# Kernel tuning notes

Hardware: AMD Instinct MI355X
Metric: run time of the kernel (lower is better)

The kernel has to match this reference:

```python
import jax, jax.numpy as jnp
import numpy as np

B, D_IN, D_H, W_RANK, U_RANK = 8192, 1024, 2048, 256, 256


def setup_inputs() -> dict:
    key = jax.random.key(0)
    ks = jax.random.split(key, 6)
    return {
        "input": jax.random.normal(ks[0], (B, D_IN), dtype=jnp.float32),
        "state": jax.random.normal(ks[1], (B, D_H), dtype=jnp.float32),
        "W1": 0.1 * jax.random.normal(ks[2], (W_RANK, D_IN), dtype=jnp.float32),
        "W2": 0.1 * jax.random.normal(ks[3], (D_H, W_RANK), dtype=jnp.float32),
        "U1": 0.1 * jax.random.normal(ks[4], (U_RANK, D_H), dtype=jnp.float32),
        "U2": 0.1 * jax.random.normal(ks[5], (D_H, U_RANK), dtype=jnp.float32),
        "bias_gate": jnp.ones((1, D_H), dtype=jnp.float32),
        "bias_update": jnp.ones((1, D_H), dtype=jnp.float32),
        "zeta": 1.0 * jnp.ones((1, 1), dtype=jnp.float32),
        "nu": -4.0 * jnp.ones((1, 1), dtype=jnp.float32),
    }


def reference(input, state, W1, W2, U1, U2, bias_gate, bias_update, zeta, nu):
    # Low-rank projections: Wx = x @ W1^T @ W2^T ; Uh = h @ U1^T @ U2^T
    wx = jnp.einsum("bi,ri->br", input, W1)          # [B, wRank]
    wx = jnp.einsum("br,hr->bh", wx, W2)             # [B, H]
    uh = jnp.einsum("bh,rh->br", state, U1)          # [B, uRank]
    uh = jnp.einsum("br,hr->bh", uh, U2)             # [B, H]
    pre = wx + uh                                     # shared pre-activation
    z = jax.nn.sigmoid(pre + bias_gate)               # gate (sigmoid)
    h_cand = jnp.tanh(pre + bias_update)              # update (tanh)
    # h_t = z*h_{t-1} + (sigmoid(zeta)*(1-z) + sigmoid(nu)) * h_cand
    new_h = z * state + (jax.nn.sigmoid(zeta) * (1.0 - z) + jax.nn.sigmoid(nu)) * h_cand
    return new_h
```

## Files before the change

### kernel.cpp

```cpp
#include <hip/hip_runtime.h>
#include <hip/hip_fp16.h>
#include <cstdint>
#include <cstddef>


typedef _Float16 half8 __attribute__((ext_vector_type(8)));
typedef float f32x4 __attribute__((ext_vector_type(4)));

#define DIN 1024
#define DH 2048
#define RK 256
#define RBLD 768
#define OFF_W1H 0
#define OFF_U1H 262144
#define OFF_W2H 786432
#define OFF_U2H 1310720

__device__ __forceinline__ half8 cvt8(const float4 a, const float4 b) {
  half8 h;
  h[0] = (_Float16)a.x; h[1] = (_Float16)a.y; h[2] = (_Float16)a.z; h[3] = (_Float16)a.w;
  h[4] = (_Float16)b.x; h[5] = (_Float16)b.y; h[6] = (_Float16)b.z; h[7] = (_Float16)b.w;
  return h;
}

__device__ __forceinline__ void gload16(const _Float16* g, _Float16* lds) {
  __builtin_amdgcn_global_load_lds(
      (const __attribute__((address_space(1))) unsigned*)g,
      (__attribute__((address_space(3))) unsigned*)lds, 16, 0, 0);
}

__global__ __launch_bounds__(256)
void fgrnn_prep(const float* __restrict__ W1, const float* __restrict__ U1,
                const float* __restrict__ W2, const float* __restrict__ U2,
                _Float16* __restrict__ wb) {
  const int q = blockIdx.x * 256 + threadIdx.x;
  const float* src;
  int rel;
  if (q < 65536) { src = W1; rel = q; }
  else if (q < 196608) { src = U1; rel = q - 65536; }
  else if (q < 327680) { src = W2; rel = q - 196608; }
  else { src = U2; rel = q - 327680; }
  const float4 v = reinterpret_cast<const float4*>(src)[rel];
  union { _Float16 h[4]; uint2 u; } cv;
  cv.h[0] = (_Float16)v.x; cv.h[1] = (_Float16)v.y;
  cv.h[2] = (_Float16)v.z; cv.h[3] = (_Float16)v.w;
  reinterpret_cast<uint2*>(wb)[q] = cv.u;
}

template <int MI>
__device__ __forceinline__ void s1_body(
    const float* __restrict__ A, const int KA, const int kbase,
    const _Float16* __restrict__ Bw, _Float16* __restrict__ rbuf,
    const int row0, const int colbase,
    _Float16* __restrict__ AsB, _Float16* __restrict__ BsB) {
  constexpr int ASTR = MI * 64 * 64;

  const int tid = threadIdx.x;
  const int lane = tid & 63;
  const int wv = tid >> 6;
  const int wr = wv >> 1, wc = wv & 1;
  const int sr = tid >> 3;
  const int sc = (tid & 7) * 8;

  f32x4 acc[MI][4];
#pragma unroll
  for (int i = 0; i < MI; ++i)
#pragma unroll
    for (int j = 0; j < 4; ++j) acc[i][j] = (f32x4){0.f, 0.f, 0.f, 0.f};

  float4 ra[MI][2];

  auto LOADA = [&](int it) {
    const int k0 = kbase + it * 64;
#pragma unroll
    for (int j = 0; j < MI; ++j) {
      const float* s = A + (size_t)(row0 + j * 64 + sr) * KA + k0 + sc;
      ra[j][0] = *reinterpret_cast<const float4*>(s);
      ra[j][1] = *reinterpret_cast<const float4*>(s + 4);
    }
  };
  auto GLOADB = [&](_Float16* bs, int it) {
    const int k0 = kbase + it * 64;
#pragma unroll
    for (int g = 0; g < 2; ++g) {
      const int rb = wv * 16 + g * 8;
      const int row = rb + (lane >> 3);
      const int ch = ((lane & 7) * 8) ^ ((row & 7) << 3);
      gload16(Bw + (size_t)row * KA + k0 + ch, bs + rb * 64);
    }
  };
  auto STOREA = [&](_Float16* as) {
#pragma unroll
    for (int j = 0; j < MI; ++j) {
      const int r = j * 64 + sr;
      *reinterpret_cast<half8*>(&as[r * 64 + (sc ^ ((r & 7) << 3))]) =
          cvt8(ra[j][0], ra[j][1]);
    }
  };
  auto COMPUTE = [&](const _Float16* as, const _Float16* bs) {
#pragma unroll
    for (int kk = 0; kk < 64; kk += 32) {
      half8 af[MI], bf[4];
#pragma unroll
      for (int mi = 0; mi < MI; ++mi) {
        const int r = wr * (MI * 16) + mi * 16 + (lane & 15);
        af[mi] = *reinterpret_cast<const half8*>(
            &as[r * 64 + ((kk + 8 * (lane >> 4)) ^ ((r & 7) << 3))]);
      }
#pragma unroll
      for (int ni = 0; ni < 4; ++ni) {
        const int r = wc * 64 + ni * 16 + (lane & 15);
        bf[ni] = *reinterpret_cast<const half8*>(
            &bs[r * 64 + ((kk + 8 * (lane >> 4)) ^ ((r & 7) << 3))]);
      }
#pragma unroll
      for (int mi = 0; mi < MI; ++mi)
#pragma unroll
        for (int ni = 0; ni < 4; ++ni)
          acc[mi][ni] =
              __builtin_amdgcn_mfma_f32_16x16x32_f16(af[mi], bf[ni], acc[mi][ni], 0, 0, 0);
    }
  };

  _Float16* as0 = AsB;
  _Float16* as1 = AsB + ASTR;
  _Float16* bs0 = BsB;
  _Float16* bs1 = BsB + 128 * 64;

  LOADA(0);
  GLOADB(bs0, 0);
  STOREA(as0);
  asm volatile("s_waitcnt vmcnt(0)" ::: "memory");
  asm volatile("s_waitcnt lgkmcnt(0)" ::: "memory");
  __builtin_amdgcn_s_barrier();
  __builtin_amdgcn_sched_barrier(0);

  int p = 0;
#pragma unroll 1
  for (int it = 0; it < 16; ++it) {
    const bool more = (it + 1 < 16);
    if (more) {
      LOADA(it + 1);
      GLOADB(p ? bs0 : bs1, it + 1);
    }
    __builtin_amdgcn_s_setprio(1);
    COMPUTE(p ? as1 : as0, p ? bs1 : bs0);
    __builtin_amdgcn_s_setprio(0);
    if (more) STOREA(p ? as0 : as1);
    asm volatile("s_waitcnt vmcnt(0)" ::: "memory");
    asm volatile("s_waitcnt lgkmcnt(0)" ::: "memory");
    __builtin_amdgcn_s_barrier();
    __builtin_amdgcn_sched_barrier(0);
    p ^= 1;
  }

#pragma unroll
  for (int mi = 0; mi < MI; ++mi)
#pragma unroll
    for (int ni = 0; ni < 4; ++ni)
#pragma unroll
      for (int e = 0; e < 4; ++e) {
        const int row = row0 + wr * (MI * 16) + mi * 16 + 4 * (lane >> 4) + e;
        const int col = colbase + wc * 64 + ni * 16 + (lane & 15);
        rbuf[(size_t)row * RBLD + col] = (_Float16)acc[mi][ni][e];
      }
}

__global__ __launch_bounds__(512)
void fgrnn_stage1(const float* __restrict__ x, const float* __restrict__ h,
                  const _Float16* __restrict__ wb, _Float16* __restrict__ rbuf) {
  __shared__ _Float16 As[2 * 256 * 64];
  __shared__ _Float16 Bs[2 * 128 * 64];
  const int bid = blockIdx.x;
  if (bid < 128) {
    const int mtile = bid >> 1;
    const int ncol = bid & 1;
    s1_body<2>(x, DIN, 0, wb + OFF_W1H + (size_t)(ncol * 128) * DIN, rbuf,
               mtile * 128, ncol * 128, As, Bs);
  } else {
    const int t = bid - 128;
    const int mtile = t >> 2;
    const int kp = (t >> 1) & 1;
    const int ncol = t & 1;
    s1_body<4>(h, DH, kp * 1024, wb + OFF_U1H + (size_t)(ncol * 128) * DH, rbuf,
               mtile * 256, 256 + kp * 256 + ncol * 128, As, Bs);
  }
}

__global__ __launch_bounds__(256)
void fgrnn_stage2(const _Float16* __restrict__ rbuf, const _Float16* __restrict__ wb,
                  const float* __restrict__ state,
                  const float* __restrict__ bg, const float* __restrict__ bu,
                  const float* __restrict__ zeta, const float* __restrict__ nu,
                  float* __restrict__ out) {
  const int bid = blockIdx.x;
  const int L = (bid & 7) * 256 + (bid >> 3);
  const int mtile = L >> 4;
  const int ntile = L & 15;
  const int row0 = mtile * 64;
  const int col0 = ntile * 128;
  const _Float16* W2h = wb + OFF_W2H;
  const _Float16* U2h = wb + OFF_U2H;

  __shared__ _Float16 As[2 * 64 * 64];
  __shared__ _Float16 Bs[2 * 128 * 64];

  const int tid = threadIdx.x;
  const int lane = tid & 63;
  const int wv = tid >> 6;
  const int wr = wv >> 1, wc = wv & 1;
  const int sr = tid >> 3;
  const int sc = (tid & 7) * 8;

  f32x4 acc[2][4];
#pragma unroll
  for (int i = 0; i < 2; ++i)
#pragma unroll
    for (int j = 0; j < 4; ++j) acc[i][j] = (f32x4){0.f, 0.f, 0.f, 0.f};

  half8 pa[2], pa2[2];

  auto LOADA = [&](int it) {
    const int k0 = it * 64;
    const bool iswx = (k0 < 256);
#pragma unroll
    for (int j = 0; j < 2; ++j) {
      const _Float16* p = rbuf + (size_t)(row0 + j * 32 + sr) * RBLD + k0 + sc;
      pa[j] = *reinterpret_cast<const half8*>(p);
      if (!iswx) pa2[j] = *reinterpret_cast<const half8*>(p + 256);
    }
  };
  auto GLOADB = [&](_Float16* bs, int it) {
    const int k0 = it * 64;
    const _Float16* Bh = (k0 < 256) ? W2h : U2h;
    const int kb = k0 & 255;
#pragma unroll
    for (int g = 0; g < 4; ++g) {
      const int rb = wv * 32 + g * 8;
      const int row = rb + (lane >> 3);
      const int ch = ((lane & 7) * 8) ^ ((row & 7) << 3);
      gload16(Bh + (size_t)(col0 + row) * RK + kb + ch, bs + rb * 64);
    }
  };
  auto STOREA = [&](_Float16* as, int it) {
    const int k0 = it * 64;
#pragma unroll
    for (int j = 0; j < 2; ++j) {
      half8 v = pa[j];
      if (k0 >= 256) v = v + pa2[j];
      const int r = j * 32 + sr;
      *reinterpret_cast<half8*>(&as[r * 64 + (sc ^ ((r & 7) << 3))]) = v;
    }
  };
  auto COMPUTE = [&](const _Float16* as, const _Float16* bs) {
#pragma unroll
    for (int kk = 0; kk < 64; kk += 32) {
      half8 af[2], bf[4];
#pragma unroll
      for (int mi = 0; mi < 2; ++mi) {
        const int r = wr * 32 + mi * 16 + (lane & 15);
        af[mi] = *reinterpret_cast<const half8*>(
            &as[r * 64 + ((kk + 8 * (lane >> 4)) ^ ((r & 7) << 3))]);
      }
#pragma unroll
      for (int ni = 0; ni < 4; ++ni) {
        const int r = wc * 64 + ni * 16 + (lane & 15);
        bf[ni] = *reinterpret_cast<const half8*>(
            &bs[r * 64 + ((kk + 8 * (lane >> 4)) ^ ((r & 7) << 3))]);
      }
#pragma unroll
      for (int mi = 0; mi < 2; ++mi)
#pragma unroll
        for (int ni = 0; ni < 4; ++ni)
          acc[mi][ni] =
              __builtin_amdgcn_mfma_f32_16x16x32_f16(af[mi], bf[ni], acc[mi][ni], 0, 0, 0);
    }
  };

  _Float16* as0 = As;
  _Float16* as1 = As + 64 * 64;
  _Float16* bs0 = Bs;
  _Float16* bs1 = Bs + 128 * 64;

  LOADA(0);
  GLOADB(bs0, 0);
  STOREA(as0, 0);
  asm volatile("s_waitcnt vmcnt(0)" ::: "memory");
  asm volatile("s_waitcnt lgkmcnt(0)" ::: "memory");
  __builtin_amdgcn_s_barrier();
  __builtin_amdgcn_sched_barrier(0);

  int p = 0;
#pragma unroll 1
  for (int it = 0; it < 8; ++it) {
    const bool more = (it + 1 < 8);
    if (more) {
      LOADA(it + 1);
      GLOADB(p ? bs0 : bs1, it + 1);
    }
    __builtin_amdgcn_s_setprio(1);
    COMPUTE(p ? as1 : as0, p ? bs1 : bs0);
    __builtin_amdgcn_s_setprio(0);
    if (more) STOREA(p ? as0 : as1, it + 1);
    asm volatile("s_waitcnt vmcnt(0)" ::: "memory");
    asm volatile("s_waitcnt lgkmcnt(0)" ::: "memory");
    __builtin_amdgcn_s_barrier();
    __builtin_amdgcn_sched_barrier(0);
    p ^= 1;
  }

  const float LOG2E = 1.44269504f;
  const float sz = __builtin_amdgcn_rcpf(1.f + __builtin_amdgcn_exp2f(-zeta[0] * LOG2E));
  const float sn = __builtin_amdgcn_rcpf(1.f + __builtin_amdgcn_exp2f(-nu[0] * LOG2E));
#pragma unroll
  for (int mi = 0; mi < 2; ++mi)
#pragma unroll
    for (int ni = 0; ni < 4; ++ni) {
      const int col = col0 + wc * 64 + ni * 16 + (lane & 15);
      const float bgc = bg[col];
      const float buc = bu[col];
#pragma unroll
      for (int e = 0; e < 4; ++e) {
        const int row = row0 + wr * 32 + mi * 16 + 4 * (lane >> 4) + e;
        const float pre = acc[mi][ni][e];
        const float zg =
            __builtin_amdgcn_rcpf(1.f + __builtin_amdgcn_exp2f(-(pre + bgc) * LOG2E));
        const float hc =
            1.f - 2.f * __builtin_amdgcn_rcpf(
                            1.f + __builtin_amdgcn_exp2f((pre + buc) * (2.f * LOG2E)));
        const float sv = state[(size_t)row * DH + col];
        out[(size_t)row * DH + col] = zg * sv + (sz * (1.f - zg) + sn) * hc;
      }
    }
}

extern "C" void kernel_launch(void* const* d_in, const int* in_sizes, int n_in,
                              void* d_out, int out_size, void* d_ws, size_t ws_size,
                              hipStream_t stream) {
  const float* input = (const float*)d_in[0];
  const float* state = (const float*)d_in[1];
  const float* W1 = (const float*)d_in[2];
  const float* W2 = (const float*)d_in[3];
  const float* U1 = (const float*)d_in[4];
  const float* U2 = (const float*)d_in[5];
  const float* bg = (const float*)d_in[6];
  const float* bu = (const float*)d_in[7];
  const float* zeta = (const float*)d_in[8];
  const float* nu = (const float*)d_in[9];
  float* out = (float*)d_out;

  _Float16* rbuf = (_Float16*)d_ws;
  _Float16* wb = rbuf + (size_t)8192 * RBLD;

  fgrnn_prep<<<1792, 256, 0, stream>>>(W1, U1, W2, U2, wb);
  fgrnn_stage1<<<256, 512, 0, stream>>>(input, state, wb, rbuf);
  fgrnn_stage2<<<2048, 256, 0, stream>>>(rbuf, wb, state, bg, bu, zeta, nu, out);
}
```

Baseline: 84.74 us.

## Prefetch stage1 A two iterations ahead; single-buffer stage2 with register staging

Stage1 now keeps two register sets for the fp32 A tile so global loads run two k-iterations ahead. It replaces the full vmcnt(0) drain with a counted wait, and A loads use nontemporal hints. Stage2 drops its double-buffered LDS and global_load_lds path for single-buffered LDS fed through registers with __syncthreads. It also adds nontemporal loads of state and stores of out. The aim is to hide stage1 load latency and stream stage2 traffic, at the cost of more registers and, in stage2, more barriers with less overlap.

```diff
diff --git a/kernel.cpp b/kernel.cpp
--- a/kernel.cpp
+++ b/kernel.cpp
@@ -16,10 +16,10 @@
 #define OFF_W2H 786432
 #define OFF_U2H 1310720
 
-__device__ __forceinline__ half8 cvt8(const float4 a, const float4 b) {
+__device__ __forceinline__ half8 cvt8(f32x4 a, f32x4 b) {
   half8 h;
-  h[0] = (_Float16)a.x; h[1] = (_Float16)a.y; h[2] = (_Float16)a.z; h[3] = (_Float16)a.w;
-  h[4] = (_Float16)b.x; h[5] = (_Float16)b.y; h[6] = (_Float16)b.z; h[7] = (_Float16)b.w;
+  h[0] = (_Float16)a[0]; h[1] = (_Float16)a[1]; h[2] = (_Float16)a[2]; h[3] = (_Float16)a[3];
+  h[4] = (_Float16)b[0]; h[5] = (_Float16)b[1]; h[6] = (_Float16)b[2]; h[7] = (_Float16)b[3];
   return h;
 }
 
@@ -68,15 +68,16 @@
 #pragma unroll
     for (int j = 0; j < 4; ++j) acc[i][j] = (f32x4){0.f, 0.f, 0.f, 0.f};
 
-  float4 ra[MI][2];
-
-  auto LOADA = [&](int it) {
+  f32x4 raE[MI][2], raO[MI][2];
+
+  auto LOADA = [&](f32x4 (&ra)[MI][2], int it) {
     const int k0 = kbase + it * 64;
 #pragma unroll
     for (int j = 0; j < MI; ++j) {
-      const float* s = A + (size_t)(row0 + j * 64 + sr) * KA + k0 + sc;
-      ra[j][0] = *reinterpret_cast<const float4*>(s);
-      ra[j][1] = *reinterpret_cast<const float4*>(s + 4);
+      const f32x4* s =
+          reinterpret_cast<const f32x4*>(A + (size_t)(row0 + j * 64 + sr) * KA + k0 + sc);
+      ra[j][0] = __builtin_nontemporal_load(s);
+      ra[j][1] = __builtin_nontemporal_load(s + 1);
     }
   };
   auto GLOADB = [&](_Float16* bs, int it) {
@@ -89,7 +90,7 @@
       gload16(Bw + (size_t)row * KA + k0 + ch, bs + rb * 64);
     }
   };
-  auto STOREA = [&](_Float16* as) {
+  auto STOREA = [&](const f32x4 (&ra)[MI][2], _Float16* as) {
 #pragma unroll
     for (int j = 0; j < MI; ++j) {
       const int r = j * 64 + sr;
@@ -121,37 +122,51 @@
               __builtin_amdgcn_mfma_f32_16x16x32_f16(af[mi], bf[ni], acc[mi][ni], 0, 0, 0);
     }
   };
+  auto WAIT_COUNTED = [&]() {
+    if constexpr (MI == 2)
+      asm volatile("s_waitcnt vmcnt(4)" ::: "memory");
+    else
+      asm volatile("s_waitcnt vmcnt(8)" ::: "memory");
+  };
 
   _Float16* as0 = AsB;
   _Float16* as1 = AsB + ASTR;
   _Float16* bs0 = BsB;
   _Float16* bs1 = BsB + 128 * 64;
 
-  LOADA(0);
   GLOADB(bs0, 0);
-  STOREA(as0);
+  LOADA(raE, 0);
+  LOADA(raO, 1);
+  STOREA(raE, as0);
   asm volatile("s_waitcnt vmcnt(0)" ::: "memory");
   asm volatile("s_waitcnt lgkmcnt(0)" ::: "memory");
   __builtin_amdgcn_s_barrier();
   __builtin_amdgcn_sched_barrier(0);
 
-  int p = 0;
 #pragma unroll 1
   for (int it = 0; it < 16; ++it) {
-    const bool more = (it + 1 < 16);
-    if (more) {
-      LOADA(it + 1);
-      GLOADB(p ? bs0 : bs1, it + 1);
+    const bool more1 = (it + 1 < 16);
+    const bool more2 = (it + 2 < 16);
+    const bool even = ((it & 1) == 0);
+    _Float16* cas = even ? as0 : as1;
+    _Float16* cbs = even ? bs0 : bs1;
+    _Float16* nas = even ? as1 : as0;
+    _Float16* nbs = even ? bs1 : bs0;
+    if (more1) GLOADB(nbs, it + 1);
+    if (more2) {
+      if (even) LOADA(raE, it + 2); else LOADA(raO, it + 2);
     }
     __builtin_amdgcn_s_setprio(1);
-    COMPUTE(p ? as1 : as0, p ? bs1 : bs0);
+    COMPUTE(cas, cbs);
     __builtin_amdgcn_s_setprio(0);
-    if (more) STOREA(p ? as0 : as1);
-    asm volatile("s_waitcnt vmcnt(0)" ::: "memory");
+    if (more1) {
+      if (even) STOREA(raO, nas); else STOREA(raE, nas);
+    }
+    if (more2) WAIT_COUNTED();
+    else asm volatile("s_waitcnt vmcnt(0)" ::: "memory");
     asm volatile("s_waitcnt lgkmcnt(0)" ::: "memory");
     __builtin_amdgcn_s_barrier();
     __builtin_amdgcn_sched_barrier(0);
-    p ^= 1;
   }
 
 #pragma unroll
@@ -202,25 +217,26 @@
   const _Float16* W2h = wb + OFF_W2H;
   const _Float16* U2h = wb + OFF_U2H;
 
-  __shared__ _Float16 As[2 * 64 * 64];
-  __shared__ _Float16 Bs[2 * 128 * 64];
+  __shared__ _Float16 As[64 * 64];
+  __shared__ _Float16 Bs[128 * 64];
 
   const int tid = threadIdx.x;
   const int lane = tid & 63;
-  const int wv = tid >> 6;
-  const int wr = wv >> 1, wc = wv & 1;
+  const int w = tid >> 6;
+  const int wr = w >> 1, wc = w & 1;
+
+  f32x4 acc[2][4];
+#pragma unroll
+  for (int i = 0; i < 2; ++i)
+#pragma unroll
+    for (int j = 0; j < 4; ++j) acc[i][j] = (f32x4){0.f, 0.f, 0.f, 0.f};
+
   const int sr = tid >> 3;
   const int sc = (tid & 7) * 8;
 
-  f32x4 acc[2][4];
-#pragma unroll
-  for (int i = 0; i < 2; ++i)
-#pragma unroll
-    for (int j = 0; j < 4; ++j) acc[i][j] = (f32x4){0.f, 0.f, 0.f, 0.f};
-
-  half8 pa[2], pa2[2];
-
-  auto LOADA = [&](int it) {
+  half8 pa[2], pa2[2], pb[4];
+
+  auto LOADG = [&](int it) {
     const int k0 = it * 64;
     const bool iswx = (k0 < 256);
 #pragma unroll
@@ -229,30 +245,35 @@
       pa[j] = *reinterpret_cast<const half8*>(p);
       if (!iswx) pa2[j] = *reinterpret_cast<const half8*>(p + 256);
     }
-  };
-  auto GLOADB = [&](_Float16* bs, int it) {
-    const int k0 = it * 64;
-    const _Float16* Bh = (k0 < 256) ? W2h : U2h;
+    const _Float16* Bh = iswx ? W2h : U2h;
     const int kb = k0 & 255;
 #pragma unroll
-    for (int g = 0; g < 4; ++g) {
-      const int rb = wv * 32 + g * 8;
-      const int row = rb + (lane >> 3);
-      const int ch = ((lane & 7) * 8) ^ ((row & 7) << 3);
-      gload16(Bh + (size_t)(col0 + row) * RK + kb + ch, bs + rb * 64);
-    }
-  };
-  auto STOREA = [&](_Float16* as, int it) {
+    for (int j = 0; j < 4; ++j)
+      pb[j] = *reinterpret_cast<const half8*>(Bh + (size_t)(col0 + j * 32 + sr) * RK + kb + sc);
+  };
+  auto STORE = [&](int it) {
     const int k0 = it * 64;
 #pragma unroll
     for (int j = 0; j < 2; ++j) {
       half8 v = pa[j];
       if (k0 >= 256) v = v + pa2[j];
       const int r = j * 32 + sr;
-      *reinterpret_cast<half8*>(&as[r * 64 + (sc ^ ((r & 7) << 3))]) = v;
-    }
-  };
-  auto COMPUTE = [&](const _Float16* as, const _Float16* bs) {
+      *reinterpret_cast<half8*>(&As[r * 64 + (sc ^ ((r & 7) << 3))]) = v;
+    }
+#pragma unroll
+    for (int j = 0; j < 4; ++j) {
+      const int r = j * 32 + sr;
+      *reinterpret_cast<half8*>(&Bs[r * 64 + (sc ^ ((r & 7) << 3))]) = pb[j];
+    }
+  };
+
+  LOADG(0);
+  STORE(0);
+  __syncthreads();
+
+  for (int it = 0; it < 8; ++it) {
+    const bool more = (it + 1 < 8);
+    if (more) LOADG(it + 1);
 #pragma unroll
     for (int kk = 0; kk < 64; kk += 32) {
       half8 af[2], bf[4];
@@ -260,13 +281,13 @@
       for (int mi = 0; mi < 2; ++mi) {
         const int r = wr * 32 + mi * 16 + (lane & 15);
         af[mi] = *reinterpret_cast<const half8*>(
-            &as[r * 64 + ((kk + 8 * (lane >> 4)) ^ ((r & 7) << 3))]);
+            &As[r * 64 + ((kk + 8 * (lane >> 4)) ^ ((r & 7) << 3))]);
       }
 #pragma unroll
       for (int ni = 0; ni < 4; ++ni) {
         const int r = wc * 64 + ni * 16 + (lane & 15);
         bf[ni] = *reinterpret_cast<const half8*>(
-            &bs[r * 64 + ((kk + 8 * (lane >> 4)) ^ ((r & 7) << 3))]);
+            &Bs[r * 64 + ((kk + 8 * (lane >> 4)) ^ ((r & 7) << 3))]);
       }
 #pragma unroll
       for (int mi = 0; mi < 2; ++mi)
@@ -275,38 +296,11 @@
           acc[mi][ni] =
               __builtin_amdgcn_mfma_f32_16x16x32_f16(af[mi], bf[ni], acc[mi][ni], 0, 0, 0);
     }
-  };
-
-  _Float16* as0 = As;
-  _Float16* as1 = As + 64 * 64;
-  _Float16* bs0 = Bs;
-  _Float16* bs1 = Bs + 128 * 64;
-
-  LOADA(0);
-  GLOADB(bs0, 0);
-  STOREA(as0, 0);
-  asm volatile("s_waitcnt vmcnt(0)" ::: "memory");
-  asm volatile("s_waitcnt lgkmcnt(0)" ::: "memory");
-  __builtin_amdgcn_s_barrier();
-  __builtin_amdgcn_sched_barrier(0);
-
-  int p = 0;
-#pragma unroll 1
-  for (int it = 0; it < 8; ++it) {
-    const bool more = (it + 1 < 8);
     if (more) {
-      LOADA(it + 1);
-      GLOADB(p ? bs0 : bs1, it + 1);
-    }
-    __builtin_amdgcn_s_setprio(1);
-    COMPUTE(p ? as1 : as0, p ? bs1 : bs0);
-    __builtin_amdgcn_s_setprio(0);
-    if (more) STOREA(p ? as0 : as1, it + 1);
-    asm volatile("s_waitcnt vmcnt(0)" ::: "memory");
-    asm volatile("s_waitcnt lgkmcnt(0)" ::: "memory");
-    __builtin_amdgcn_s_barrier();
-    __builtin_amdgcn_sched_barrier(0);
-    p ^= 1;
+      __syncthreads();
+      STORE(it + 1);
+    }
+    __syncthreads();
   }
 
   const float LOG2E = 1.44269504f;
@@ -328,8 +322,9 @@
         const float hc =
             1.f - 2.f * __builtin_amdgcn_rcpf(
                             1.f + __builtin_amdgcn_exp2f((pre + buc) * (2.f * LOG2E)));
-        const float sv = state[(size_t)row * DH + col];
-        out[(size_t)row * DH + col] = zg * sv + (sz * (1.f - zg) + sn) * hc;
+        const float sv = __builtin_nontemporal_load(&state[(size_t)row * DH + col]);
+        __builtin_nontemporal_store(zg * sv + (sz * (1.f - zg) + sn) * hc,
+                                    &out[(size_t)row * DH + col]);
       }
     }
 }
```

Result: slower. 127.0 us (+49.9%).
